# Kernel optimization log

Measured on AMD Instinct MI355X. Metric: run time of the kernel, lower is better.

Reference implementation:

```python
import jax, jax.numpy as jnp
import numpy as np

DIM, HEADS = 512, 8
CH = DIM // HEADS  # 64
WINDOWS = [3, 5, 7]
HEAD_SPLITS = [2, 3, 3]  # heads per conv window group (sums to HEADS)


def setup_inputs() -> dict:
    key = jax.random.key(0)
    ks = jax.random.split(key, 12)
    B, N = 8, 4096
    s = 0.02
    inp = {
        'x':  jax.random.normal(ks[0], (B, N, DIM), jnp.float32),
        'mx': jax.random.normal(ks[1], (B, N, DIM), jnp.float32),
        'Wqkv': jax.random.normal(ks[2], (3 * DIM, DIM), jnp.float32) * s,
        'Wproj': jax.random.normal(ks[3], (DIM, DIM), jnp.float32) * s,
        'bproj': jax.random.normal(ks[4], (DIM,), jnp.float32) * s,
        'Wmix': jax.random.normal(ks[5], (CH, 2 * CH), jnp.float32) * s,
        'bmix': jax.random.normal(ks[6], (CH,), jnp.float32) * s,
    }
    for i, (w, hs) in enumerate(zip(WINDOWS, HEAD_SPLITS)):
        gc = hs * CH  # depthwise channels in this group
        inp[f'conv_w{w}'] = jax.random.normal(ks[7 + i], (gc, 1, w, w), jnp.float32) * s
        inp[f'conv_b{w}'] = jnp.zeros((gc,), jnp.float32)
    inp['H'] = 64
    inp['W'] = 64
    return inp


def _dwconv(x, w, b, k):
    # x: [B, C, H, W]; depthwise conv, 'same' padding
    out = jax.lax.conv_general_dilated(
        x, w, window_strides=(1, 1), padding=[(k // 2, k // 2)] * 2,
        feature_group_count=x.shape[1],
        dimension_numbers=('NCHW', 'OIHW', 'NCHW'))
    return out + b[None, :, None, None]


def _crpe(q, v, H, W, conv_ws, conv_bs):
    # q, v: [B, h, N, Ch] with N == H*W
    B, h, N, ch = q.shape
    v_img = v.transpose(0, 1, 3, 2).reshape(B, h * ch, H, W)
    bounds = np.cumsum([0] + [s * ch for s in HEAD_SPLITS])
    outs = [_dwconv(v_img[:, bounds[i]:bounds[i + 1]], conv_ws[i], conv_bs[i], WINDOWS[i])
            for i in range(len(WINDOWS))]
    conv_v = jnp.concatenate(outs, axis=1).reshape(B, h, ch, H * W).transpose(0, 1, 3, 2)
    return q * conv_v


def reference(x, mx, Wqkv, Wproj, bproj, Wmix, bmix,
              conv_w3, conv_w5, conv_w7, conv_b3, conv_b5, conv_b7, H, W):
    B, N, C = x.shape
    scale = CH ** -0.5
    # qkv for x: [B,N,3C] -> [3,B,h,N,Ch]
    qkv = (x @ Wqkv.T).reshape(B, N, 3, HEADS, CH).transpose(2, 0, 3, 1, 4)
    q, k, v = qkv[0], qkv[1], qkv[2]
    # only the q-part of qkv(mx) is used
    mq = (mx @ Wqkv[:C].T).reshape(B, N, HEADS, CH).transpose(0, 2, 1, 3)
    # mixed q (fed to crpe only)
    q_mix = jnp.concatenate([mq, q], axis=-1) @ Wmix.T + bmix
    # factorized attention: softmax over sequence dim of k
    k_sm = jax.nn.softmax(k, axis=2)
    kv = jnp.einsum('bhnk,bhnv->bhkv', k_sm, v)          # [B,h,Ch,Ch]
    factor_att = jnp.einsum('bhnk,bhkv->bhnv', mq, kv)    # [B,h,N,Ch]
    crpe = _crpe(q_mix, v, H, W,
                 (conv_w3, conv_w5, conv_w7), (conv_b3, conv_b5, conv_b7))
    out = scale * factor_att + crpe
    out = out.transpose(0, 2, 1, 3).reshape(B, N, C)
    return out @ Wproj.T + bproj
```

## Files before the change

### kernel.cpp

```cpp
#include <hip/hip_runtime.h>
#include <hip/hip_bf16.h>

#define MROWS 32768
#define NSEQ 4096
#define KDIM 512

typedef short sh8 __attribute__((ext_vector_type(8)));
typedef float fx4 __attribute__((ext_vector_type(4)));

__device__ __forceinline__ unsigned short f2bf(float f) {
  union { float f; unsigned u; } v; v.f = f;
  unsigned r = v.u + 0x7FFFu + ((v.u >> 16) & 1u);
  return (unsigned short)(r >> 16);
}
__device__ __forceinline__ float bf2f(unsigned short u) {
  union { unsigned u; float f; } v; v.u = ((unsigned)u) << 16;
  return v.f;
}

template<bool A_BF16, bool OUT_BF16, bool HAS_BIAS, bool TWO, bool PER_B2, bool W2_BF16>
__global__ __launch_bounds__(256) void gemm_mfma(
    const void* Av, const float* __restrict__ W,
    const void* A2v, const void* W2v,
    const float* __restrict__ bias, void* Co, int Nn) {
  __shared__ unsigned short As[128][40];
  __shared__ unsigned short Bs[128][40];
  const int tid = threadIdx.x;
  const int lane = tid & 63, wv = tid >> 6;
  const int wr = wv >> 1, wc = wv & 1;
  const int bx = blockIdx.x, by = blockIdx.y;
  const int fr = lane & 15, fg = lane >> 4;
  fx4 acc[4][4] = {};
#pragma unroll
  for (int pass = 0; pass < (TWO ? 2 : 1); ++pass) {
    const void* Ap = (TWO && pass) ? A2v : Av;
    for (int k0 = 0; k0 < KDIM; k0 += 32) {
      if constexpr (A_BF16) {
        const unsigned short* Ab = (const unsigned short*)Ap;
#pragma unroll
        for (int s = 0; s < 2; ++s) {
          int idx = s * 256 + tid;
          int r = idx >> 2, kq = idx & 3;
          *reinterpret_cast<uint4*>(&As[r][kq * 8]) =
              *reinterpret_cast<const uint4*>(Ab + (size_t)(by * 128 + r) * KDIM + k0 + kq * 8);
        }
      } else {
        const float* Af = (const float*)Ap;
#pragma unroll
        for (int s = 0; s < 4; ++s) {
          int idx = s * 256 + tid;
          int r = idx >> 3, kq = idx & 7;
          float4 v = *reinterpret_cast<const float4*>(
              Af + (size_t)(by * 128 + r) * KDIM + k0 + kq * 4);
          ushort4 o;
          o.x = f2bf(v.x); o.y = f2bf(v.y); o.z = f2bf(v.z); o.w = f2bf(v.w);
          *reinterpret_cast<ushort4*>(&As[r][kq * 4]) = o;
        }
      }
      if (W2_BF16 && TWO && pass) {
        const unsigned short* Wb16 = (const unsigned short*)W2v;
        if constexpr (PER_B2) Wb16 += (size_t)(by >> 5) * KDIM * 512;
#pragma unroll
        for (int s = 0; s < 2; ++s) {
          int idx = s * 256 + tid;
          int r = idx >> 2, kq = idx & 3;
          *reinterpret_cast<uint4*>(&Bs[r][kq * 8]) =
              *reinterpret_cast<const uint4*>(Wb16 + (size_t)(bx * 128 + r) * KDIM + k0 + kq * 8);
        }
      } else {
        const float* Wp = (TWO && pass) ? (const float*)W2v : W;
#pragma unroll
        for (int s = 0; s < 4; ++s) {
          int idx = s * 256 + tid;
          int r = idx >> 3, kq = idx & 7;
          float4 v = *reinterpret_cast<const float4*>(
              Wp + (size_t)(bx * 128 + r) * KDIM + k0 + kq * 4);
          ushort4 o;
          o.x = f2bf(v.x); o.y = f2bf(v.y); o.z = f2bf(v.z); o.w = f2bf(v.w);
          *reinterpret_cast<ushort4*>(&Bs[r][kq * 4]) = o;
        }
      }
      __syncthreads();
      sh8 a[4], b[4];
#pragma unroll
      for (int m = 0; m < 4; ++m)
        a[m] = *reinterpret_cast<const sh8*>(&As[wr * 64 + m * 16 + fr][fg * 8]);
#pragma unroll
      for (int n = 0; n < 4; ++n)
        b[n] = *reinterpret_cast<const sh8*>(&Bs[wc * 64 + n * 16 + fr][fg * 8]);
#pragma unroll
      for (int m = 0; m < 4; ++m)
#pragma unroll
        for (int n = 0; n < 4; ++n)
          acc[m][n] = __builtin_amdgcn_mfma_f32_16x16x32_bf16(a[m], b[n], acc[m][n], 0, 0, 0);
      __syncthreads();
    }
  }
  unsigned short* Cb = (unsigned short*)Co;
  float* Cf = (float*)Co;
#pragma unroll
  for (int n = 0; n < 4; ++n) {
    int col = bx * 128 + wc * 64 + n * 16 + fr;
    float bb = 0.f;
    if constexpr (HAS_BIAS) bb = bias[col];
#pragma unroll
    for (int m = 0; m < 4; ++m) {
#pragma unroll
      for (int j = 0; j < 4; ++j) {
        int row = by * 128 + wr * 64 + m * 16 + fg * 4 + j;
        float val = acc[m][n][j] + bb;
        if constexpr (OUT_BF16)
          Cb[(size_t)row * Nn + col] = f2bf(val);
        else
          Cf[(size_t)row * Nn + col] = val;
      }
    }
  }
}

__global__ __launch_bounds__(256) void eff_weights(
    const float* __restrict__ Wqkv, const float* __restrict__ Wmix,
    const float* __restrict__ bmix,
    float* __restrict__ W1, float* __restrict__ W2,
    float* __restrict__ bmixfull) {
  int r = blockIdx.x;
  int h = r >> 6, j = r & 63;
  int t = threadIdx.x;
  if (t == 0) bmixfull[r] = bmix[j];
  float a10 = 0.f, a11 = 0.f, a20 = 0.f, a21 = 0.f;
  for (int i = 0; i < 64; ++i) {
    float w1 = Wmix[j * 128 + i], w2 = Wmix[j * 128 + 64 + i];
    const float* wr = Wqkv + (size_t)(h * 64 + i) * KDIM;
    a10 = fmaf(w1, wr[t], a10);
    a11 = fmaf(w1, wr[t + 256], a11);
    a20 = fmaf(w2, wr[t], a20);
    a21 = fmaf(w2, wr[t + 256], a21);
  }
  W1[(size_t)r * KDIM + t] = a10;
  W1[(size_t)r * KDIM + t + 256] = a11;
  W2[(size_t)r * KDIM + t] = a20;
  W2[(size_t)r * KDIM + t + 256] = a21;
}

__global__ __launch_bounds__(256) void wtrans(
    const float* __restrict__ w3, const float* __restrict__ w5,
    const float* __restrict__ w7,
    float* __restrict__ wT3, float* __restrict__ wT5, float* __restrict__ wT7) {
  int i = blockIdx.x * 256 + threadIdx.x;
  if (i < 1152) {
    int ti = i >> 7, c = i & 127;
    wT3[i] = w3[c * 9 + ti];
  } else if (i < 5952) {
    int j = i - 1152;
    int ti = j / 192, c = j - ti * 192;
    wT5[j] = w5[c * 25 + ti];
  } else {
    int j = i - 5952;
    int ti = j / 192, c = j - ti * 192;
    wT7[j] = w7[c * 49 + ti];
  }
}

__global__ __launch_bounds__(256) void zero_colsum(float* __restrict__ p) {
  int i = (blockIdx.x * 256 + threadIdx.x) * 4;
  *reinterpret_cast<float4*>(p + i) = make_float4(0.f, 0.f, 0.f, 0.f);
}

__global__ __launch_bounds__(256) void kv_mfma(
    const unsigned short* __restrict__ kvmat,
    float* __restrict__ kvpart, float* __restrict__ colsum) {
  __shared__ unsigned short eK[64][40];
  __shared__ unsigned short eV[64][40];
  __shared__ float cw[4][64];
  int t = threadIdx.x;
  int split = blockIdx.x & 7;
  int bh = blockIdx.x >> 3;
  int h = bh & 7, b = bh >> 3;
  int lane = t & 63, wv = t >> 6;
  int wr = wv >> 1, wc = wv & 1;
  int fr = lane & 15, fg = lane >> 4;
  int cg = t & 7, nl = t >> 3;
  const unsigned short* kb = kvmat + (size_t)b * NSEQ * 1024 + h * 64 + cg * 8;
  const unsigned short* vb = kb + 512;
  int colS = nl ^ ((cg & 3) << 3);
  fx4 acc[2][2] = {};
  float csum[8] = {};
  for (int n0 = split * 512; n0 < split * 512 + 512; n0 += 32) {
    size_t off = (size_t)(n0 + nl) * 1024;
    sh8 k8 = *reinterpret_cast<const sh8*>(kb + off);
    sh8 v8 = *reinterpret_cast<const sh8*>(vb + off);
#pragma unroll
    for (int j = 0; j < 8; ++j) {
      float e = __expf(bf2f((unsigned short)k8[j]));
      csum[j] += e;
      eK[cg * 8 + j][colS] = f2bf(e);
      eV[cg * 8 + j][colS] = (unsigned short)v8[j];
    }
    __syncthreads();
    sh8 a[2], bb[2];
#pragma unroll
    for (int m = 0; m < 2; ++m) {
      int r = wr * 32 + m * 16 + fr;
      int c8 = (fg ^ ((r >> 3) & 3)) * 8;
      a[m] = *reinterpret_cast<const sh8*>(&eK[r][c8]);
    }
#pragma unroll
    for (int n = 0; n < 2; ++n) {
      int r = wc * 32 + n * 16 + fr;
      int c8 = (fg ^ ((r >> 3) & 3)) * 8;
      bb[n] = *reinterpret_cast<const sh8*>(&eV[r][c8]);
    }
#pragma unroll
    for (int m = 0; m < 2; ++m)
#pragma unroll
      for (int n = 0; n < 2; ++n)
        acc[m][n] = __builtin_amdgcn_mfma_f32_16x16x32_bf16(a[m], bb[n], acc[m][n], 0, 0, 0);
    __syncthreads();
  }
  float* kvp = kvpart + (size_t)split * 64 * 4096 + (size_t)bh * 4096;
#pragma unroll
  for (int m = 0; m < 2; ++m)
#pragma unroll
    for (int n = 0; n < 2; ++n)
#pragma unroll
      for (int j = 0; j < 4; ++j) {
        int row = wr * 32 + m * 16 + fg * 4 + j;
        int col = wc * 32 + n * 16 + fr;
        kvp[row * 64 + col] = acc[m][n][j];
      }
#pragma unroll
  for (int j = 0; j < 8; ++j) {
    float v = csum[j];
    v += __shfl_xor(v, 8);
    v += __shfl_xor(v, 16);
    v += __shfl_xor(v, 32);
    csum[j] = v;
  }
  if (lane < 8) {
#pragma unroll
    for (int j = 0; j < 8; ++j) cw[wv][lane * 8 + j] = csum[j];
  }
  __syncthreads();
  if (t < 64) {
    float s = cw[0][t] + cw[1][t] + cw[2][t] + cw[3][t];
    atomicAdd(&colsum[b * 512 + h * 64 + t], s);
  }
}

__global__ __launch_bounds__(256) void kv_reduce(
    const float* __restrict__ kvpart, float* __restrict__ kvbuf) {
  int i = (blockIdx.x * 256 + threadIdx.x) * 4;
  float4 s = make_float4(0.f, 0.f, 0.f, 0.f);
#pragma unroll
  for (int sp = 0; sp < 8; ++sp) {
    float4 v = *reinterpret_cast<const float4*>(kvpart + (size_t)sp * 262144 + i);
    s.x += v.x; s.y += v.y; s.z += v.z; s.w += v.w;
  }
  *reinterpret_cast<float4*>(kvbuf + i) = s;
}

__global__ __launch_bounds__(256) void wproj_eff(
    const float* __restrict__ kvbuf, const float* __restrict__ Wproj,
    const float* __restrict__ colsum, unsigned short* __restrict__ Wb) {
  int bid = blockIdx.x;
  int jt = bid & 15, h = (bid >> 4) & 7, b = bid >> 7;
  int j0 = jt * 32;
  __shared__ float kvs[64][65];
  __shared__ float wps[32][64];
  int t = threadIdx.x;
  const float* kvsrc = kvbuf + (size_t)(b * 8 + h) * 4096;
  for (int i = t; i < 4096; i += 256) kvs[i >> 6][i & 63] = kvsrc[i];
  for (int i = t; i < 2048; i += 256)
    wps[i >> 6][i & 63] = Wproj[(size_t)(j0 + (i >> 6)) * 512 + h * 64 + (i & 63)];
  __syncthreads();
  int ck = t & 63, jl = t >> 6;
  float rs = 0.125f / colsum[b * 512 + h * 64 + ck];
  float acc[8] = {};
  for (int ch = 0; ch < 64; ++ch) {
    float kvv = kvs[ck][ch];
#pragma unroll
    for (int g = 0; g < 8; ++g)
      acc[g] = fmaf(kvv, wps[jl * 8 + g][ch], acc[g]);
  }
#pragma unroll
  for (int g = 0; g < 8; ++g)
    Wb[((size_t)b * 512 + j0 + jl * 8 + g) * 512 + h * 64 + ck] = f2bf(rs * acc[g]);
}

template<int KW, int C0, int CG, int TPB>
__global__ __launch_bounds__(TPB) void conv_crpe(
    const unsigned short* __restrict__ kvmat,
    unsigned short* __restrict__ qmixb,
    const float* __restrict__ wT, const float* __restrict__ bias) {
  constexpr int SLOTS = CG / 8;
  constexpr int ROWS_PB = TPB / SLOTS;
  constexpr int P = KW / 2;
  int t = threadIdx.x;
  int row_local = t / SLOTS;
  int slot = t - row_local * SLOTS;
  int row = blockIdx.x * ROWS_PB + row_local;
  int n = row & 4095, b = row >> 12;
  int y = n >> 6, x = n & 63;
  int cl = slot * 8;
  float acc[8] = {};
  const unsigned short* vb =
      kvmat + (size_t)b * NSEQ * 1024 + 512 + C0 + cl;
#pragma unroll
  for (int dy = 0; dy < KW; ++dy) {
    int yy = y + dy - P;
    if ((unsigned)yy >= 64u) continue;
#pragma unroll
    for (int dx = 0; dx < KW; ++dx) {
      int xq = x + dx - P;
      if ((unsigned)xq >= 64u) continue;
      sh8 v8 = *reinterpret_cast<const sh8*>(vb + (size_t)(yy * 64 + xq) * 1024);
      const float* wp = wT + (dy * KW + dx) * CG + cl;
      float4 w0 = *reinterpret_cast<const float4*>(wp);
      float4 w1 = *reinterpret_cast<const float4*>(wp + 4);
      acc[0] = fmaf(w0.x, bf2f((unsigned short)v8[0]), acc[0]);
      acc[1] = fmaf(w0.y, bf2f((unsigned short)v8[1]), acc[1]);
      acc[2] = fmaf(w0.z, bf2f((unsigned short)v8[2]), acc[2]);
      acc[3] = fmaf(w0.w, bf2f((unsigned short)v8[3]), acc[3]);
      acc[4] = fmaf(w1.x, bf2f((unsigned short)v8[4]), acc[4]);
      acc[5] = fmaf(w1.y, bf2f((unsigned short)v8[5]), acc[5]);
      acc[6] = fmaf(w1.z, bf2f((unsigned short)v8[6]), acc[6]);
      acc[7] = fmaf(w1.w, bf2f((unsigned short)v8[7]), acc[7]);
    }
  }
  float4 b0 = *reinterpret_cast<const float4*>(bias + cl);
  float4 b1 = *reinterpret_cast<const float4*>(bias + cl + 4);
  unsigned short* qp = qmixb + (size_t)row * 512 + C0 + cl;
  sh8 qm = *reinterpret_cast<const sh8*>(qp);
  sh8 out;
  out[0] = (short)f2bf(bf2f((unsigned short)qm[0]) * (acc[0] + b0.x));
  out[1] = (short)f2bf(bf2f((unsigned short)qm[1]) * (acc[1] + b0.y));
  out[2] = (short)f2bf(bf2f((unsigned short)qm[2]) * (acc[2] + b0.z));
  out[3] = (short)f2bf(bf2f((unsigned short)qm[3]) * (acc[3] + b0.w));
  out[4] = (short)f2bf(bf2f((unsigned short)qm[4]) * (acc[4] + b1.x));
  out[5] = (short)f2bf(bf2f((unsigned short)qm[5]) * (acc[5] + b1.y));
  out[6] = (short)f2bf(bf2f((unsigned short)qm[6]) * (acc[6] + b1.z));
  out[7] = (short)f2bf(bf2f((unsigned short)qm[7]) * (acc[7] + b1.w));
  *reinterpret_cast<sh8*>(qp) = out;
}

extern "C" void kernel_launch(void* const* d_in, const int* in_sizes, int n_in,
                              void* d_out, int out_size, void* d_ws, size_t ws_size,
                              hipStream_t stream) {
  const float* x     = (const float*)d_in[0];
  const float* mx    = (const float*)d_in[1];
  const float* Wqkv  = (const float*)d_in[2];
  const float* Wproj = (const float*)d_in[3];
  const float* bproj = (const float*)d_in[4];
  const float* Wmix  = (const float*)d_in[5];
  const float* bmix  = (const float*)d_in[6];
  const float* w3    = (const float*)d_in[7];
  const float* b3    = (const float*)d_in[8];
  const float* w5    = (const float*)d_in[9];
  const float* b5    = (const float*)d_in[10];
  const float* w7    = (const float*)d_in[11];
  const float* b7    = (const float*)d_in[12];

  unsigned short* kvmat = (unsigned short*)d_out;

  char* wsp = (char*)d_ws;
  auto carve = [&wsp](size_t bytes) {
    char* p = wsp;
    wsp += (bytes + 255) & ~(size_t)255;
    return p;
  };
  unsigned short* mqb   = (unsigned short*)carve((size_t)MROWS * 512 * 2);
  unsigned short* qmixb = (unsigned short*)carve((size_t)MROWS * 512 * 2);
  float* W1     = (float*)carve(512 * 512 * 4);
  float* W2     = (float*)carve(512 * 512 * 4);
  float* bmixf  = (float*)carve(512 * 4);
  float* kvbuf  = (float*)carve(8 * 8 * 64 * 64 * 4);
  float* colsum = (float*)carve(4096 * 4);
  float* wT3    = (float*)carve(9 * 128 * 4);
  float* wT5    = (float*)carve(25 * 192 * 4);
  float* wT7    = (float*)carve(49 * 192 * 4);
  float* kvpart = (float*)carve((size_t)8 * 64 * 4096 * 4);
  unsigned short* Wb = (unsigned short*)carve((size_t)8 * 512 * 512 * 2);

  dim3 blk(256);
  eff_weights<<<dim3(512), blk, 0, stream>>>(Wqkv, Wmix, bmix, W1, W2, bmixf);
  wtrans<<<dim3(60), blk, 0, stream>>>(w3, w5, w7, wT3, wT5, wT7);
  gemm_mfma<false, true, false, false, false, false><<<dim3(8, 256), blk, 0, stream>>>(
      x, Wqkv + (size_t)512 * 512, nullptr, nullptr, nullptr, kvmat, 1024);
  gemm_mfma<false, true, false, false, false, false><<<dim3(4, 256), blk, 0, stream>>>(
      mx, Wqkv, nullptr, nullptr, nullptr, mqb, 512);
  gemm_mfma<false, true, true, true, false, false><<<dim3(4, 256), blk, 0, stream>>>(
      mx, W1, x, W2, bmixf, qmixb, 512);
  zero_colsum<<<dim3(4), blk, 0, stream>>>(colsum);
  kv_mfma<<<dim3(512), blk, 0, stream>>>(kvmat, kvpart, colsum);
  kv_reduce<<<dim3(256), blk, 0, stream>>>(kvpart, kvbuf);
  wproj_eff<<<dim3(1024), blk, 0, stream>>>(kvbuf, Wproj, colsum, Wb);
  conv_crpe<3, 0, 128, 256><<<dim3(2048), dim3(256), 0, stream>>>(kvmat, qmixb, wT3, b3);
  conv_crpe<5, 128, 192, 192><<<dim3(4096), dim3(192), 0, stream>>>(kvmat, qmixb, wT5, b5);
  conv_crpe<7, 320, 192, 192><<<dim3(4096), dim3(192), 0, stream>>>(kvmat, qmixb, wT7, b7);
  gemm_mfma<true, false, true, true, true, true><<<dim3(4, 256), blk, 0, stream>>>(
      qmixb, Wproj, mqb, Wb, bproj, d_out, 512);
}
```

Before: 618.0 us.

## Rework GEMM with bf16 weights, direct-to-LDS loads, swizzled LDS, and tile remap

Weights are converted to bf16 once up front, and the fused effective weights are now stored as bf16. The GEMM kernel loads bf16 tiles straight from global memory into LDS with global_load_lds and uses an XOR-swizzled 64-wide K tile to avoid bank conflicts. It also halves the number of K iterations and remaps the 1D grid so neighbouring workgroups share tiles in cache. The goal is to cut redundant fp32 weight conversion, LDS bank conflicts and loop overhead in the projection GEMMs, at the cost of two extra conversion launches and more LDS per block.

```diff
diff --git a/kernel.cpp b/kernel.cpp
--- a/kernel.cpp
+++ b/kernel.cpp
@@ -18,81 +18,92 @@
   return v.f;
 }
 
-template<bool A_BF16, bool OUT_BF16, bool HAS_BIAS, bool TWO, bool PER_B2, bool W2_BF16>
-__global__ __launch_bounds__(256) void gemm_mfma(
-    const void* Av, const float* __restrict__ W,
-    const void* A2v, const void* W2v,
+__device__ __forceinline__ void gload16(const unsigned short* g, unsigned short* l) {
+  __builtin_amdgcn_global_load_lds(
+      (const __attribute__((address_space(1))) unsigned int*)g,
+      (__attribute__((address_space(3))) unsigned int*)l, 16, 0, 0);
+}
+
+template<bool A_BF16, bool OUT_BF16, bool HAS_BIAS, bool TWO, bool PER_B2, int NXL>
+__global__ __launch_bounds__(256) void gemm_bf16(
+    const void* Av, const unsigned short* __restrict__ W,
+    const void* A2v, const unsigned short* __restrict__ W2,
     const float* __restrict__ bias, void* Co, int Nn) {
-  __shared__ unsigned short As[128][40];
-  __shared__ unsigned short Bs[128][40];
+  __shared__ unsigned short As[128 * 64];
+  __shared__ unsigned short Bs[128 * 64];
   const int tid = threadIdx.x;
   const int lane = tid & 63, wv = tid >> 6;
   const int wr = wv >> 1, wc = wv & 1;
-  const int bx = blockIdx.x, by = blockIdx.y;
+  const int nwg = gridDim.x;
+  const int lid = (blockIdx.x & 7) * (nwg >> 3) + (blockIdx.x >> 3);
+  const int bx = lid & ((1 << NXL) - 1);
+  const int by = lid >> NXL;
   const int fr = lane & 15, fg = lane >> 4;
+  const int srow = lane >> 3;
+  const int sphys = lane & 7;
   fx4 acc[4][4] = {};
 #pragma unroll
   for (int pass = 0; pass < (TWO ? 2 : 1); ++pass) {
+    const unsigned short* Wp = (TWO && pass) ? W2 : W;
+    if (TWO && pass && PER_B2) Wp += (size_t)(by >> 5) * (512 * 512);
     const void* Ap = (TWO && pass) ? A2v : Av;
-    for (int k0 = 0; k0 < KDIM; k0 += 32) {
+    for (int k0 = 0; k0 < KDIM; k0 += 64) {
+#pragma unroll
+      for (int l = 0; l < 4; ++l) {
+        int rb = wv * 4 + l;
+        int r = rb * 8 + srow;
+        int clog = sphys ^ (r & 7);
+        gload16(Wp + (size_t)(bx * 128 + r) * KDIM + k0 + clog * 8, &Bs[rb * 512]);
+      }
       if constexpr (A_BF16) {
         const unsigned short* Ab = (const unsigned short*)Ap;
 #pragma unroll
-        for (int s = 0; s < 2; ++s) {
-          int idx = s * 256 + tid;
-          int r = idx >> 2, kq = idx & 3;
-          *reinterpret_cast<uint4*>(&As[r][kq * 8]) =
-              *reinterpret_cast<const uint4*>(Ab + (size_t)(by * 128 + r) * KDIM + k0 + kq * 8);
+        for (int l = 0; l < 4; ++l) {
+          int rb = wv * 4 + l;
+          int r = rb * 8 + srow;
+          int clog = sphys ^ (r & 7);
+          gload16(Ab + (size_t)(by * 128 + r) * KDIM + k0 + clog * 8, &As[rb * 512]);
         }
       } else {
         const float* Af = (const float*)Ap;
 #pragma unroll
         for (int s = 0; s < 4; ++s) {
-          int idx = s * 256 + tid;
-          int r = idx >> 3, kq = idx & 7;
-          float4 v = *reinterpret_cast<const float4*>(
-              Af + (size_t)(by * 128 + r) * KDIM + k0 + kq * 4);
-          ushort4 o;
-          o.x = f2bf(v.x); o.y = f2bf(v.y); o.z = f2bf(v.z); o.w = f2bf(v.w);
-          *reinterpret_cast<ushort4*>(&As[r][kq * 4]) = o;
-        }
-      }
-      if (W2_BF16 && TWO && pass) {
-        const unsigned short* Wb16 = (const unsigned short*)W2v;
-        if constexpr (PER_B2) Wb16 += (size_t)(by >> 5) * KDIM * 512;
-#pragma unroll
-        for (int s = 0; s < 2; ++s) {
-          int idx = s * 256 + tid;
-          int r = idx >> 2, kq = idx & 3;
-          *reinterpret_cast<uint4*>(&Bs[r][kq * 8]) =
-              *reinterpret_cast<const uint4*>(Wb16 + (size_t)(bx * 128 + r) * KDIM + k0 + kq * 8);
-        }
-      } else {
-        const float* Wp = (TWO && pass) ? (const float*)W2v : W;
-#pragma unroll
-        for (int s = 0; s < 4; ++s) {
-          int idx = s * 256 + tid;
-          int r = idx >> 3, kq = idx & 7;
-          float4 v = *reinterpret_cast<const float4*>(
-              Wp + (size_t)(bx * 128 + r) * KDIM + k0 + kq * 4);
-          ushort4 o;
-          o.x = f2bf(v.x); o.y = f2bf(v.y); o.z = f2bf(v.z); o.w = f2bf(v.w);
-          *reinterpret_cast<ushort4*>(&Bs[r][kq * 4]) = o;
+          int u = s * 256 + tid;
+          int r = u >> 3, cp = u & 7;
+          int clog = cp ^ (r & 7);
+          const float* src = Af + (size_t)(by * 128 + r) * KDIM + k0 + clog * 8;
+          float4 v0 = *reinterpret_cast<const float4*>(src);
+          float4 v1 = *reinterpret_cast<const float4*>(src + 4);
+          uint4 o;
+          o.x = (unsigned)f2bf(v0.x) | ((unsigned)f2bf(v0.y) << 16);
+          o.y = (unsigned)f2bf(v0.z) | ((unsigned)f2bf(v0.w) << 16);
+          o.z = (unsigned)f2bf(v1.x) | ((unsigned)f2bf(v1.y) << 16);
+          o.w = (unsigned)f2bf(v1.z) | ((unsigned)f2bf(v1.w) << 16);
+          *reinterpret_cast<uint4*>(&As[r * 64 + cp * 8]) = o;
         }
       }
       __syncthreads();
-      sh8 a[4], b[4];
-#pragma unroll
-      for (int m = 0; m < 4; ++m)
-        a[m] = *reinterpret_cast<const sh8*>(&As[wr * 64 + m * 16 + fr][fg * 8]);
-#pragma unroll
-      for (int n = 0; n < 4; ++n)
-        b[n] = *reinterpret_cast<const sh8*>(&Bs[wc * 64 + n * 16 + fr][fg * 8]);
-#pragma unroll
-      for (int m = 0; m < 4; ++m)
-#pragma unroll
-        for (int n = 0; n < 4; ++n)
-          acc[m][n] = __builtin_amdgcn_mfma_f32_16x16x32_bf16(a[m], b[n], acc[m][n], 0, 0, 0);
+#pragma unroll
+      for (int ks = 0; ks < 2; ++ks) {
+        sh8 a[4], b[4];
+#pragma unroll
+        for (int m = 0; m < 4; ++m) {
+          int r = wr * 64 + m * 16 + fr;
+          int p = (ks * 4 + fg) ^ (r & 7);
+          a[m] = *reinterpret_cast<const sh8*>(&As[r * 64 + p * 8]);
+        }
+#pragma unroll
+        for (int n = 0; n < 4; ++n) {
+          int r = wc * 64 + n * 16 + fr;
+          int p = (ks * 4 + fg) ^ (r & 7);
+          b[n] = *reinterpret_cast<const sh8*>(&Bs[r * 64 + p * 8]);
+        }
+#pragma unroll
+        for (int m = 0; m < 4; ++m)
+#pragma unroll
+          for (int n = 0; n < 4; ++n)
+            acc[m][n] = __builtin_amdgcn_mfma_f32_16x16x32_bf16(a[m], b[n], acc[m][n], 0, 0, 0);
+      }
       __syncthreads();
     }
   }
@@ -118,10 +129,24 @@
   }
 }
 
+__global__ __launch_bounds__(256) void cvt_bf16(
+    const float* __restrict__ src, unsigned short* __restrict__ dst, int n8) {
+  int i = blockIdx.x * 256 + threadIdx.x;
+  if (i >= n8) return;
+  float4 v0 = *reinterpret_cast<const float4*>(src + (size_t)i * 8);
+  float4 v1 = *reinterpret_cast<const float4*>(src + (size_t)i * 8 + 4);
+  uint4 o;
+  o.x = (unsigned)f2bf(v0.x) | ((unsigned)f2bf(v0.y) << 16);
+  o.y = (unsigned)f2bf(v0.z) | ((unsigned)f2bf(v0.w) << 16);
+  o.z = (unsigned)f2bf(v1.x) | ((unsigned)f2bf(v1.y) << 16);
+  o.w = (unsigned)f2bf(v1.z) | ((unsigned)f2bf(v1.w) << 16);
+  *reinterpret_cast<uint4*>(dst + (size_t)i * 8) = o;
+}
+
 __global__ __launch_bounds__(256) void eff_weights(
     const float* __restrict__ Wqkv, const float* __restrict__ Wmix,
     const float* __restrict__ bmix,
-    float* __restrict__ W1, float* __restrict__ W2,
+    unsigned short* __restrict__ W1, unsigned short* __restrict__ W2,
     float* __restrict__ bmixfull) {
   int r = blockIdx.x;
   int h = r >> 6, j = r & 63;
@@ -136,10 +161,10 @@
     a20 = fmaf(w2, wr[t], a20);
     a21 = fmaf(w2, wr[t + 256], a21);
   }
-  W1[(size_t)r * KDIM + t] = a10;
-  W1[(size_t)r * KDIM + t + 256] = a11;
-  W2[(size_t)r * KDIM + t] = a20;
-  W2[(size_t)r * KDIM + t + 256] = a21;
+  W1[(size_t)r * KDIM + t] = f2bf(a10);
+  W1[(size_t)r * KDIM + t + 256] = f2bf(a11);
+  W2[(size_t)r * KDIM + t] = f2bf(a20);
+  W2[(size_t)r * KDIM + t + 256] = f2bf(a21);
 }
 
 __global__ __launch_bounds__(256) void wtrans(
@@ -368,10 +393,12 @@
     wsp += (bytes + 255) & ~(size_t)255;
     return p;
   };
-  unsigned short* mqb   = (unsigned short*)carve((size_t)MROWS * 512 * 2);
-  unsigned short* qmixb = (unsigned short*)carve((size_t)MROWS * 512 * 2);
-  float* W1     = (float*)carve(512 * 512 * 4);
-  float* W2     = (float*)carve(512 * 512 * 4);
+  unsigned short* mqb    = (unsigned short*)carve((size_t)MROWS * 512 * 2);
+  unsigned short* qmixb  = (unsigned short*)carve((size_t)MROWS * 512 * 2);
+  unsigned short* Wqkvb  = (unsigned short*)carve((size_t)1536 * 512 * 2);
+  unsigned short* Wprojb = (unsigned short*)carve((size_t)512 * 512 * 2);
+  unsigned short* W1b    = (unsigned short*)carve((size_t)512 * 512 * 2);
+  unsigned short* W2b    = (unsigned short*)carve((size_t)512 * 512 * 2);
   float* bmixf  = (float*)carve(512 * 4);
   float* kvbuf  = (float*)carve(8 * 8 * 64 * 64 * 4);
   float* colsum = (float*)carve(4096 * 4);
@@ -382,14 +409,16 @@
   unsigned short* Wb = (unsigned short*)carve((size_t)8 * 512 * 512 * 2);
 
   dim3 blk(256);
-  eff_weights<<<dim3(512), blk, 0, stream>>>(Wqkv, Wmix, bmix, W1, W2, bmixf);
+  eff_weights<<<dim3(512), blk, 0, stream>>>(Wqkv, Wmix, bmix, W1b, W2b, bmixf);
   wtrans<<<dim3(60), blk, 0, stream>>>(w3, w5, w7, wT3, wT5, wT7);
-  gemm_mfma<false, true, false, false, false, false><<<dim3(8, 256), blk, 0, stream>>>(
-      x, Wqkv + (size_t)512 * 512, nullptr, nullptr, nullptr, kvmat, 1024);
-  gemm_mfma<false, true, false, false, false, false><<<dim3(4, 256), blk, 0, stream>>>(
-      mx, Wqkv, nullptr, nullptr, nullptr, mqb, 512);
-  gemm_mfma<false, true, true, true, false, false><<<dim3(4, 256), blk, 0, stream>>>(
-      mx, W1, x, W2, bmixf, qmixb, 512);
+  cvt_bf16<<<dim3(384), blk, 0, stream>>>(Wqkv, Wqkvb, 1536 * 512 / 8);
+  cvt_bf16<<<dim3(128), blk, 0, stream>>>(Wproj, Wprojb, 512 * 512 / 8);
+  gemm_bf16<false, true, false, false, false, 3><<<dim3(2048), blk, 0, stream>>>(
+      x, Wqkvb + (size_t)512 * 512, nullptr, nullptr, nullptr, kvmat, 1024);
+  gemm_bf16<false, true, false, false, false, 2><<<dim3(1024), blk, 0, stream>>>(
+      mx, Wqkvb, nullptr, nullptr, nullptr, mqb, 512);
+  gemm_bf16<false, true, true, true, false, 2><<<dim3(1024), blk, 0, stream>>>(
+      mx, W1b, x, W2b, bmixf, qmixb, 512);
   zero_colsum<<<dim3(4), blk, 0, stream>>>(colsum);
   kv_mfma<<<dim3(512), blk, 0, stream>>>(kvmat, kvpart, colsum);
   kv_reduce<<<dim3(256), blk, 0, stream>>>(kvpart, kvbuf);
@@ -397,6 +426,6 @@
   conv_crpe<3, 0, 128, 256><<<dim3(2048), dim3(256), 0, stream>>>(kvmat, qmixb, wT3, b3);
   conv_crpe<5, 128, 192, 192><<<dim3(4096), dim3(192), 0, stream>>>(kvmat, qmixb, wT5, b5);
   conv_crpe<7, 320, 192, 192><<<dim3(4096), dim3(192), 0, stream>>>(kvmat, qmixb, wT7, b7);
-  gemm_mfma<true, false, true, true, true, true><<<dim3(4, 256), blk, 0, stream>>>(
-      qmixb, Wproj, mqb, Wb, bproj, d_out, 512);
-}
+  gemm_bf16<true, false, true, true, true, 2><<<dim3(1024), blk, 0, stream>>>(
+      qmixb, Wprojb, mqb, Wb, bproj, d_out, 512);
+}
```

Measured after the change: 551.7 us. -10.7%, faster.
